# Optimization experiments

Hardware: AMD Instinct MI355X
Metric: run time of the kernel (lower is better)

The kernel has to match this reference:

```python
import jax, jax.numpy as jnp
import numpy as np

NEG_BIG = -2.0**32 + 1.0

def setup_inputs() -> dict:
    key = jax.random.key(0)
    ks = jax.random.split(key, 8)
    B, T, D = 4096, 200, 32
    H1, H2 = 80, 40
    s = lambda n: 1.0 / np.sqrt(n)
    return {
        "q": jax.random.normal(ks[0], (B, D), jnp.float32),
        "k": jax.random.normal(ks[1], (B, T, D), jnp.float32),
        "v": jax.random.normal(ks[2], (B, T, D), jnp.float32),
        "mask": jax.random.randint(ks[3], (B, T), 0, 2, jnp.int32),
        "Wq": jax.random.normal(ks[4], (D, D), jnp.float32) * s(D),
        "bq": jnp.zeros((D,), jnp.float32),
        "alpha": jnp.zeros((D,), jnp.float32),  # Keras PReLU default alpha=0
        "W1": jax.random.normal(ks[5], (4 * D, H1), jnp.float32) * s(4 * D),
        "b1": jnp.zeros((H1,), jnp.float32),
        "W2": jax.random.normal(ks[6], (H1, H2), jnp.float32) * s(H1),
        "b2": jnp.zeros((H2,), jnp.float32),
        "Wf": jax.random.normal(ks[7], (H2, 1), jnp.float32) * s(H2),
        "bf": jnp.zeros((1,), jnp.float32),
    }

def prelu(x, a):
    return jnp.where(x >= 0, x, a * x)

def reference(q, k, v, mask, Wq, bq, alpha, W1, b1, W2, b2, Wf, bf):
    # dense_q with PReLU activation: [B, D] -> [B, 32]
    qp = prelu(q @ Wq + bq, alpha)
    # tile query across history steps: [B, T, 32]
    qt = jnp.broadcast_to(qp[:, None, :], k.shape)
    # DIN attention features: [B, T, 4*32]
    info = jnp.concatenate([qt, k, qt - k, qt * k], axis=-1)
    info = jax.nn.sigmoid(info @ W1 + b1)
    info = jax.nn.sigmoid(info @ W2 + b2)
    logits = (info @ Wf + bf).squeeze(-1)  # [B, T]
    logits = jnp.where(mask == 0, jnp.full_like(logits, NEG_BIG), logits)
    att = jax.nn.softmax(logits, axis=-1)
    return att[:, None, :]  # [B, 1, T]
```

## Files before the change

kernel.cpp:

```cpp
#include <hip/hip_runtime.h>
#include <math.h>

typedef float f32x4 __attribute__((ext_vector_type(4)));
typedef _Float16 f16;
typedef f16 f16x8 __attribute__((ext_vector_type(8)));
typedef unsigned int u32;
typedef u32 u32x2 __attribute__((ext_vector_type(2)));

#define BB 4096
#define TT 200
#define DD 32
#define H1 80
#define H2 40
#define SLAB_W 104
#define LOG2E 1.44269504f

__device__ __align__(16) float g_BCj[DD * H1];
__device__ __align__(16) float g_Dj [DD * H1];
__device__ __align__(16) float g_ACj[DD * H1];
__device__ __align__(16) f16 g_w2h[9 * 64 * 8];

__device__ __forceinline__ float exp2_raw(float x) {
    float r;
    asm("v_exp_f32 %0, %1" : "=v"(r) : "v"(x));
    return r;
}
__device__ __forceinline__ float sig_pre(float a) {
    return __builtin_amdgcn_rcpf(1.f + exp2_raw(a));
}

__global__ void pack_kernel(const float* __restrict__ W1, const float* __restrict__ W2) {
    int idx = blockIdx.x * 256 + threadIdx.x;
    if (idx < DD * H1) {
        int kk = idx / H1, j = idx % H1;
        g_BCj[idx] = -LOG2E * (W1[(32 + kk) * H1 + j] - W1[(64 + kk) * H1 + j]);
        g_Dj [idx] = -LOG2E * W1[(96 + kk) * H1 + j];
        g_ACj[idx] = -LOG2E * (W1[kk * H1 + j] + W1[(64 + kk) * H1 + j]);
        return;
    }
    idx -= DD * H1;
    if (idx < 9 * 64 * 8) {
        int e = idx & 7, l = (idx >> 3) & 63, g = idx >> 9;
        int kt = g / 3, n = g % 3;
        int j   = kt * 32 + (l >> 4) * 8 + e;
        int col = n * 16 + (l & 15);
        float v = (j < H1 && col < H2) ? W2[j * H2 + col] : 0.f;
        g_w2h[idx] = (f16)(-LOG2E * v);
    }
}

__global__ __launch_bounds__(256) void din_mfma(
    const float* __restrict__ q, const float* __restrict__ k, const int* __restrict__ mask,
    const float* __restrict__ Wq, const float* __restrict__ bq, const float* __restrict__ alpha,
    const float* __restrict__ b1, const float* __restrict__ b2, const float* __restrict__ Wf,
    float* __restrict__ out)
{
    const int tid = threadIdx.x;
    const int wid = tid >> 6, l = tid & 63;
    const int l15 = l & 15, lg4 = l >> 4;
    const int r   = wid >> 1, s = wid & 1;
    const int b   = (blockIdx.x << 1) | r;

    __shared__ __align__(16) f16   slab[4][16][SLAB_W];
    __shared__ __align__(16) float qp_s[2][DD];
    __shared__ __align__(16) float u_s[2][H1];
    __shared__ __align__(16) float lgt[2][208];

    f16x8 W2r[9];
    #pragma unroll
    for (int g = 0; g < 9; ++g) W2r[g] = *(const f16x8*)(g_w2h + (g * 64 + l) * 8);

    const int* mrow = mask + (size_t)b * TT;
    int mk0 = mrow[l];
    int mk1 = mrow[64 + l];
    int mk2 = mrow[128 + l];
    int mk3 = (l < 8) ? mrow[192 + l] : 1;

    if (s == 0 && l < DD) {
        const float* qr = q + (size_t)b * DD;
        float acc = bq[l];
        #pragma unroll
        for (int e = 0; e < DD; ++e) acc += qr[e] * Wq[e * DD + l];
        float a = alpha[l];
        qp_s[r][l] = acc >= 0.f ? acc : a * acc;
    }
    {
        u32* z0 = (u32*)slab[wid];
        #pragma unroll
        for (int i = 0; i < 2; ++i) {
            int idx = i * 64 + l;
            z0[(idx >> 3) * 52 + 40 + (idx & 7)] = 0u;
        }
    }

    __syncthreads();
    const float* qp = qp_s[r];

    #pragma unroll
    for (int i = 0; i < 2; ++i) {
        int c = i * 64 + l;
        if (c < H1) {
            float acc = -LOG2E * b1[c];
            #pragma unroll
            for (int d = 0; d < DD; ++d) acc += qp[d] * g_ACj[d * H1 + c];
            u_s[r][c] = acc;
        }
    }
    f16x8 Bh[5];
    #pragma unroll
    for (int n = 0; n < 5; ++n) {
        #pragma unroll
        for (int e = 0; e < 8; ++e) {
            int kidx = lg4 * 8 + e;
            int j = n * 16 + l15;
            Bh[n][e] = (f16)(g_BCj[kidx * H1 + j] + qp[kidx] * g_Dj[kidx * H1 + j]);
        }
    }
    f32x4 b2r[3], wfr[3];
    #pragma unroll
    for (int n = 0; n < 3; ++n) {
        int c0 = n * 16 + lg4 * 4;
        if (c0 + 3 < H2) {
            f32x4 bv = *(const f32x4*)(b2 + c0);
            f32x4 wv = *(const f32x4*)(Wf + c0);
            #pragma unroll
            for (int e = 0; e < 4; ++e) { bv[e] *= -LOG2E; wv[e] *= LOG2E; }
            b2r[n] = bv;
            wfr[n] = wv;
        } else {
            b2r[n] = (f32x4){0.f, 0.f, 0.f, 0.f};
            wfr[n] = (f32x4){0.f, 0.f, 0.f, 0.f};
        }
    }
    f32x4 ur[5];
    #pragma unroll
    for (int n = 0; n < 5; ++n) ur[n] = *(const f32x4*)(&u_s[r][n * 16 + lg4 * 4]);

    const float* kb = k + (size_t)b * (TT * DD);
    f16 (*ws)[SLAB_W] = slab[wid];
    float* lg = lgt[r];

    f32x4 x0, x1;
    auto loadk = [&](int m) {
        int t = m * 16 + l15; if (t > TT - 1) t = TT - 1;
        const f32x4* kr = (const f32x4*)(kb + t * DD + lg4 * 8);
        x0 = kr[0]; x1 = kr[1];
    };

    auto l1_full = [&](int nload) {
        f16x8 Ah;
        #pragma unroll
        for (int e = 0; e < 4; ++e) {
            Ah[e]     = (f16)x0[e];
            Ah[e + 4] = (f16)x1[e];
        }
        if (nload >= 0) loadk(nload);
        #pragma unroll
        for (int n = 0; n < 5; ++n) {
            int j0 = n * 16 + lg4 * 4;
            f32x4 acc = ur[n];
            acc = __builtin_amdgcn_mfma_f32_16x16x32_f16(Bh[n], Ah, acc, 0, 0, 0);
            auto p01 = __builtin_amdgcn_cvt_pkrtz(sig_pre(acc[0]), sig_pre(acc[1]));
            auto p23 = __builtin_amdgcn_cvt_pkrtz(sig_pre(acc[2]), sig_pre(acc[3]));
            u32x2 w;
            w[0] = __builtin_bit_cast(u32, p01);
            w[1] = __builtin_bit_cast(u32, p23);
            *(u32x2*)(&ws[l15][j0]) = w;
        }
    };

    auto body = [&](int m) {
        f16x8 sh0 = *(const f16x8*)(&ws[l15][0 * 32 + lg4 * 8]);
        f16x8 sh1 = *(const f16x8*)(&ws[l15][1 * 32 + lg4 * 8]);
        f16x8 sh2 = *(const f16x8*)(&ws[l15][2 * 32 + lg4 * 8]);

        if (m + 2 < 13) l1_full(m + 4 < 13 ? m + 4 : -1);

        f32x4 a0 = {0.f,0.f,0.f,0.f}, a1 = {0.f,0.f,0.f,0.f}, a2 = {0.f,0.f,0.f,0.f};
        #pragma unroll
        for (int kt = 0; kt < 3; ++kt) {
            f16x8 sh = (kt == 0) ? sh0 : (kt == 1) ? sh1 : sh2;
            a0 = __builtin_amdgcn_mfma_f32_16x16x32_f16(W2r[kt * 3 + 0], sh, a0, 0, 0, 0);
            a1 = __builtin_amdgcn_mfma_f32_16x16x32_f16(W2r[kt * 3 + 1], sh, a1, 0, 0, 0);
            a2 = __builtin_amdgcn_mfma_f32_16x16x32_f16(W2r[kt * 3 + 2], sh, a2, 0, 0, 0);
        }

        float pn[3];
        #pragma unroll
        for (int n = 0; n < 3; ++n) {
            f32x4 av = (n == 0) ? a0 : (n == 1) ? a1 : a2;
            float t0 = wfr[n][0] * sig_pre(av[0] + b2r[n][0]);
            float t1 = wfr[n][1] * sig_pre(av[1] + b2r[n][1]);
            float t2 = wfr[n][2] * sig_pre(av[2] + b2r[n][2]);
            float t3 = wfr[n][3] * sig_pre(av[3] + b2r[n][3]);
            pn[n] = (t0 + t1) + (t2 + t3);
        }
        float p = (pn[0] + pn[1]) + pn[2];
        p += __shfl_xor(p, 16);
        p += __shfl_xor(p, 32);
        if (l < 16) lg[m * 16 + l15] = p;
    };

    loadk(s);
    l1_full(s + 2 < 13 ? s + 2 : -1);
    for (int m = s; m < 13; m += 2) body(m);

    __syncthreads();

    const float NEG = -4294967295.0f;
    float v0 = lg[l];        if (mk0 == 0) v0 = NEG;
    float v1 = lg[64 + l];   if (mk1 == 0) v1 = NEG;
    float v2 = lg[128 + l];  if (mk2 == 0) v2 = NEG;
    float v3 = -8589934590.0f;
    if (l < 8) { v3 = lg[192 + l]; if (mk3 == 0) v3 = NEG; }

    float mx = fmaxf(fmaxf(v0, v1), fmaxf(v2, v3));
    #pragma unroll
    for (int off = 32; off; off >>= 1) mx = fmaxf(mx, __shfl_xor(mx, off));

    float e0 = exp2_raw(v0 - mx), e1 = exp2_raw(v1 - mx);
    float e2 = exp2_raw(v2 - mx), e3 = exp2_raw(v3 - mx);
    float ssum = (e0 + e1) + (e2 + e3);
    #pragma unroll
    for (int off = 32; off; off >>= 1) ssum += __shfl_xor(ssum, off);

    float* orow = out + (size_t)b * TT;
    if (s == 0) {
        orow[l]      = e0 / ssum;
        orow[64 + l] = e1 / ssum;
    } else {
        orow[128 + l] = e2 / ssum;
        if (l < 8) orow[192 + l] = e3 / ssum;
    }
}

extern "C" void kernel_launch(void* const* d_in, const int* in_sizes, int n_in,
                              void* d_out, int out_size, void* d_ws, size_t ws_size,
                              hipStream_t stream) {
    const float* q     = (const float*)d_in[0];
    const float* k     = (const float*)d_in[1];
    const int*   mask  = (const int*)d_in[3];
    const float* Wq    = (const float*)d_in[4];
    const float* bq    = (const float*)d_in[5];
    const float* alpha = (const float*)d_in[6];
    const float* W1    = (const float*)d_in[7];
    const float* b1    = (const float*)d_in[8];
    const float* W2    = (const float*)d_in[9];
    const float* b2    = (const float*)d_in[10];
    const float* Wf    = (const float*)d_in[11];
    float* out = (float*)d_out;

    hipLaunchKernelGGL(pack_kernel, dim3((DD * H1 + 9 * 64 * 8 + 255) / 256), dim3(256),
                       0, stream, W1, W2);
    hipLaunchKernelGGL(din_mfma, dim3(BB / 2), dim3(256), 0, stream,
                       q, k, mask, Wq, bq, alpha, b1, b2, Wf, out);
}
```

Before: 58.60 us.

## Assign one wave per batch row with double-buffered slabs and LDS-resident W2

Each wave now owns a whole batch row, so a 256-thread block covers four rows and the grid is halved. The two-wave split per row is gone, which removes the cross-wave q projection sharing and the split softmax write. The W2 fragments and per-row layer-1 bias vectors move from registers into shared memory to relieve register pressure. Each wave interleaves two time tiles with double-buffered slabs to expose more independent MFMA and sigmoid work. The cost is extra LDS traffic for weights on every tile, and fewer blocks in flight.

```diff
diff --git a/kernel.cpp b/kernel.cpp
--- a/kernel.cpp
+++ b/kernel.cpp
@@ -58,17 +58,20 @@
     const int tid = threadIdx.x;
     const int wid = tid >> 6, l = tid & 63;
     const int l15 = l & 15, lg4 = l >> 4;
-    const int r   = wid >> 1, s = wid & 1;
-    const int b   = (blockIdx.x << 1) | r;
-
-    __shared__ __align__(16) f16   slab[4][16][SLAB_W];
-    __shared__ __align__(16) float qp_s[2][DD];
-    __shared__ __align__(16) float u_s[2][H1];
-    __shared__ __align__(16) float lgt[2][208];
-
-    f16x8 W2r[9];
-    #pragma unroll
-    for (int g = 0; g < 9; ++g) W2r[g] = *(const f16x8*)(g_w2h + (g * 64 + l) * 8);
+    const int b   = (blockIdx.x << 2) | wid;
+
+    __shared__ __align__(16) f16   slab[4][2][16][SLAB_W];
+    __shared__ __align__(16) f16   w2h_s[9 * 64 * 8];
+    __shared__ __align__(16) float u_s[4][H1];
+    __shared__ __align__(16) float lgt[4][208];
+    float* qp = lgt[wid];
+
+    {
+        const u32* src = (const u32*)g_w2h;
+        u32* dst = (u32*)w2h_s;
+        #pragma unroll
+        for (int i = 0; i < 9; ++i) dst[i * 256 + tid] = src[i * 256 + tid];
+    }
 
     const int* mrow = mask + (size_t)b * TT;
     int mk0 = mrow[l];
@@ -76,25 +79,25 @@
     int mk2 = mrow[128 + l];
     int mk3 = (l < 8) ? mrow[192 + l] : 1;
 
-    if (s == 0 && l < DD) {
+    if (l < DD) {
         const float* qr = q + (size_t)b * DD;
         float acc = bq[l];
         #pragma unroll
         for (int e = 0; e < DD; ++e) acc += qr[e] * Wq[e * DD + l];
         float a = alpha[l];
-        qp_s[r][l] = acc >= 0.f ? acc : a * acc;
+        qp[l] = acc >= 0.f ? acc : a * acc;
     }
     {
-        u32* z0 = (u32*)slab[wid];
+        u32* z0 = (u32*)slab[wid][0];
+        u32* z1 = (u32*)slab[wid][1];
         #pragma unroll
         for (int i = 0; i < 2; ++i) {
             int idx = i * 64 + l;
-            z0[(idx >> 3) * 52 + 40 + (idx & 7)] = 0u;
-        }
-    }
-
-    __syncthreads();
-    const float* qp = qp_s[r];
+            int off = (idx >> 3) * 52 + 40 + (idx & 7);
+            z0[off] = 0u;
+            z1[off] = 0u;
+        }
+    }
 
     #pragma unroll
     for (int i = 0; i < 2; ++i) {
@@ -103,7 +106,7 @@
             float acc = -LOG2E * b1[c];
             #pragma unroll
             for (int d = 0; d < DD; ++d) acc += qp[d] * g_ACj[d * H1 + c];
-            u_s[r][c] = acc;
+            u_s[wid][c] = acc;
         }
     }
     f16x8 Bh[5];
@@ -132,59 +135,55 @@
             wfr[n] = (f32x4){0.f, 0.f, 0.f, 0.f};
         }
     }
-    f32x4 ur[5];
-    #pragma unroll
-    for (int n = 0; n < 5; ++n) ur[n] = *(const f32x4*)(&u_s[r][n * 16 + lg4 * 4]);
+
+    __syncthreads();
 
     const float* kb = k + (size_t)b * (TT * DD);
-    f16 (*ws)[SLAB_W] = slab[wid];
-    float* lg = lgt[r];
-
-    f32x4 x0, x1;
-    auto loadk = [&](int m) {
+    f16 (*ws0)[SLAB_W] = slab[wid][0];
+    f16 (*ws1)[SLAB_W] = slab[wid][1];
+    float* lg = lgt[wid];
+
+    f32x4 x0, x1, x2, x3;
+    auto loadk = [&](int m, f32x4& a, f32x4& c) {
         int t = m * 16 + l15; if (t > TT - 1) t = TT - 1;
         const f32x4* kr = (const f32x4*)(kb + t * DD + lg4 * 8);
-        x0 = kr[0]; x1 = kr[1];
+        a = kr[0]; c = kr[1];
     };
 
-    auto l1_full = [&](int nload) {
+    auto l1_full = [&](f16 (*wbuf)[SLAB_W], f32x4& xa, f32x4& xb, int nload) {
         f16x8 Ah;
         #pragma unroll
         for (int e = 0; e < 4; ++e) {
-            Ah[e]     = (f16)x0[e];
-            Ah[e + 4] = (f16)x1[e];
-        }
-        if (nload >= 0) loadk(nload);
+            Ah[e]     = (f16)xa[e];
+            Ah[e + 4] = (f16)xb[e];
+        }
+        if (nload >= 0) loadk(nload, xa, xb);
         #pragma unroll
         for (int n = 0; n < 5; ++n) {
             int j0 = n * 16 + lg4 * 4;
-            f32x4 acc = ur[n];
+            f32x4 acc = *(const f32x4*)(&u_s[wid][j0]);
             acc = __builtin_amdgcn_mfma_f32_16x16x32_f16(Bh[n], Ah, acc, 0, 0, 0);
             auto p01 = __builtin_amdgcn_cvt_pkrtz(sig_pre(acc[0]), sig_pre(acc[1]));
             auto p23 = __builtin_amdgcn_cvt_pkrtz(sig_pre(acc[2]), sig_pre(acc[3]));
             u32x2 w;
             w[0] = __builtin_bit_cast(u32, p01);
             w[1] = __builtin_bit_cast(u32, p23);
-            *(u32x2*)(&ws[l15][j0]) = w;
+            *(u32x2*)(&wbuf[l15][j0]) = w;
         }
     };
 
-    auto body = [&](int m) {
-        f16x8 sh0 = *(const f16x8*)(&ws[l15][0 * 32 + lg4 * 8]);
-        f16x8 sh1 = *(const f16x8*)(&ws[l15][1 * 32 + lg4 * 8]);
-        f16x8 sh2 = *(const f16x8*)(&ws[l15][2 * 32 + lg4 * 8]);
-
-        if (m + 2 < 13) l1_full(m + 4 < 13 ? m + 4 : -1);
-
+    auto l2_one = [&](int m, f16x8 sh0, f16x8 sh1, f16x8 sh2) {
         f32x4 a0 = {0.f,0.f,0.f,0.f}, a1 = {0.f,0.f,0.f,0.f}, a2 = {0.f,0.f,0.f,0.f};
         #pragma unroll
         for (int kt = 0; kt < 3; ++kt) {
+            f16x8 w0 = *(const f16x8*)(w2h_s + ((kt * 3 + 0) * 64 + l) * 8);
+            f16x8 w1 = *(const f16x8*)(w2h_s + ((kt * 3 + 1) * 64 + l) * 8);
+            f16x8 w2 = *(const f16x8*)(w2h_s + ((kt * 3 + 2) * 64 + l) * 8);
             f16x8 sh = (kt == 0) ? sh0 : (kt == 1) ? sh1 : sh2;
-            a0 = __builtin_amdgcn_mfma_f32_16x16x32_f16(W2r[kt * 3 + 0], sh, a0, 0, 0, 0);
-            a1 = __builtin_amdgcn_mfma_f32_16x16x32_f16(W2r[kt * 3 + 1], sh, a1, 0, 0, 0);
-            a2 = __builtin_amdgcn_mfma_f32_16x16x32_f16(W2r[kt * 3 + 2], sh, a2, 0, 0, 0);
-        }
-
+            a0 = __builtin_amdgcn_mfma_f32_16x16x32_f16(w0, sh, a0, 0, 0, 0);
+            a1 = __builtin_amdgcn_mfma_f32_16x16x32_f16(w1, sh, a1, 0, 0, 0);
+            a2 = __builtin_amdgcn_mfma_f32_16x16x32_f16(w2, sh, a2, 0, 0, 0);
+        }
         float pn[3];
         #pragma unroll
         for (int n = 0; n < 3; ++n) {
@@ -201,11 +200,26 @@
         if (l < 16) lg[m * 16 + l15] = p;
     };
 
-    loadk(s);
-    l1_full(s + 2 < 13 ? s + 2 : -1);
-    for (int m = s; m < 13; m += 2) body(m);
-
-    __syncthreads();
+    loadk(0, x0, x1);
+    loadk(1, x2, x3);
+    l1_full(ws0, x0, x1, 2);
+    l1_full(ws1, x2, x3, 3);
+
+    for (int m = 0; m < 13; m += 2) {
+        f16x8 sA0 = *(const f16x8*)(&ws0[l15][0 * 32 + lg4 * 8]);
+        f16x8 sA1 = *(const f16x8*)(&ws0[l15][1 * 32 + lg4 * 8]);
+        f16x8 sA2 = *(const f16x8*)(&ws0[l15][2 * 32 + lg4 * 8]);
+        f16x8 sB0, sB1, sB2;
+        if (m + 1 < 13) {
+            sB0 = *(const f16x8*)(&ws1[l15][0 * 32 + lg4 * 8]);
+            sB1 = *(const f16x8*)(&ws1[l15][1 * 32 + lg4 * 8]);
+            sB2 = *(const f16x8*)(&ws1[l15][2 * 32 + lg4 * 8]);
+        }
+        if (m + 2 < 13) l1_full(ws0, x0, x1, (m + 4 < 13) ? m + 4 : -1);
+        if (m + 3 < 13) l1_full(ws1, x2, x3, (m + 5 < 13) ? m + 5 : -1);
+        l2_one(m, sA0, sA1, sA2);
+        if (m + 1 < 13) l2_one(m + 1, sB0, sB1, sB2);
+    }
 
     const float NEG = -4294967295.0f;
     float v0 = lg[l];        if (mk0 == 0) v0 = NEG;
@@ -225,13 +239,10 @@
     for (int off = 32; off; off >>= 1) ssum += __shfl_xor(ssum, off);
 
     float* orow = out + (size_t)b * TT;
-    if (s == 0) {
-        orow[l]      = e0 / ssum;
-        orow[64 + l] = e1 / ssum;
-    } else {
-        orow[128 + l] = e2 / ssum;
-        if (l < 8) orow[192 + l] = e3 / ssum;
-    }
+    orow[l]       = e0 / ssum;
+    orow[64 + l]  = e1 / ssum;
+    orow[128 + l] = e2 / ssum;
+    if (l < 8) orow[192 + l] = e3 / ssum;
 }
 
 extern "C" void kernel_launch(void* const* d_in, const int* in_sizes, int n_in,
@@ -252,6 +263,6 @@
 
     hipLaunchKernelGGL(pack_kernel, dim3((DD * H1 + 9 * 64 * 8 + 255) / 256), dim3(256),
                        0, stream, W1, W2);
-    hipLaunchKernelGGL(din_mfma, dim3(BB / 2), dim3(256), 0, stream,
+    hipLaunchKernelGGL(din_mfma, dim3(BB / 4), dim3(256), 0, stream,
                        q, k, mask, Wq, bq, alpha, b1, b2, Wf, out);
 }
```

After: 51.68 us. -11.8%, faster.

## Assign one batch row per wavefront and pre-pack weights for vector loads

Applied to the files above, without the earlier changes.

Each wavefront now handles a whole batch row instead of two wavefronts splitting one row's time tiles. This removes both block-wide __syncthreads and leaves each wave independent, though every wave now does the full per-row prologue (query projection, u vector, Bh build). The pack kernel now also writes a transposed Wq and lane-ordered W1 fragments, so those prologue dot products use float4 loads instead of strided scalar loads. The grid shrinks to BB/4 blocks, and per-wave serial work per block goes up.

```diff
diff --git a/kernel.cpp b/kernel.cpp
--- a/kernel.cpp
+++ b/kernel.cpp
@@ -15,10 +15,11 @@
 #define SLAB_W 104
 #define LOG2E 1.44269504f
 
-__device__ __align__(16) float g_BCj[DD * H1];
-__device__ __align__(16) float g_Dj [DD * H1];
-__device__ __align__(16) float g_ACj[DD * H1];
-__device__ __align__(16) f16 g_w2h[9 * 64 * 8];
+__device__ __align__(16) float g_wqt[DD * DD];
+__device__ __align__(16) float g_act[H1 * DD];
+__device__ __align__(16) float g_bcf[5 * 64 * 8];
+__device__ __align__(16) float g_df [5 * 64 * 8];
+__device__ __align__(16) f16   g_w2h[9 * 64 * 8];
 
 __device__ __forceinline__ float exp2_raw(float x) {
     float r;
@@ -29,16 +30,30 @@
     return __builtin_amdgcn_rcpf(1.f + exp2_raw(a));
 }
 
-__global__ void pack_kernel(const float* __restrict__ W1, const float* __restrict__ W2) {
+__global__ void pack_kernel(const float* __restrict__ W1, const float* __restrict__ W2,
+                            const float* __restrict__ Wq) {
     int idx = blockIdx.x * 256 + threadIdx.x;
-    if (idx < DD * H1) {
-        int kk = idx / H1, j = idx % H1;
-        g_BCj[idx] = -LOG2E * (W1[(32 + kk) * H1 + j] - W1[(64 + kk) * H1 + j]);
-        g_Dj [idx] = -LOG2E * W1[(96 + kk) * H1 + j];
-        g_ACj[idx] = -LOG2E * (W1[kk * H1 + j] + W1[(64 + kk) * H1 + j]);
+    if (idx < DD * DD) {
+        int col = idx / DD, e = idx % DD;
+        g_wqt[idx] = Wq[e * DD + col];
         return;
     }
-    idx -= DD * H1;
+    idx -= DD * DD;
+    if (idx < H1 * DD) {
+        int c = idx / DD, d = idx % DD;
+        g_act[idx] = -LOG2E * (W1[d * H1 + c] + W1[(64 + d) * H1 + c]);
+        return;
+    }
+    idx -= H1 * DD;
+    if (idx < 5 * 64 * 8) {
+        int e = idx & 7, l = (idx >> 3) & 63, n = idx >> 9;
+        int kidx = (l >> 4) * 8 + e;
+        int j = n * 16 + (l & 15);
+        g_bcf[idx] = -LOG2E * (W1[(32 + kidx) * H1 + j] - W1[(64 + kidx) * H1 + j]);
+        g_df [idx] = -LOG2E * W1[(96 + kidx) * H1 + j];
+        return;
+    }
+    idx -= 5 * 64 * 8;
     if (idx < 9 * 64 * 8) {
         int e = idx & 7, l = (idx >> 3) & 63, g = idx >> 9;
         int kt = g / 3, n = g % 3;
@@ -51,20 +66,19 @@
 
 __global__ __launch_bounds__(256) void din_mfma(
     const float* __restrict__ q, const float* __restrict__ k, const int* __restrict__ mask,
-    const float* __restrict__ Wq, const float* __restrict__ bq, const float* __restrict__ alpha,
+    const float* __restrict__ bq, const float* __restrict__ alpha,
     const float* __restrict__ b1, const float* __restrict__ b2, const float* __restrict__ Wf,
     float* __restrict__ out)
 {
     const int tid = threadIdx.x;
     const int wid = tid >> 6, l = tid & 63;
     const int l15 = l & 15, lg4 = l >> 4;
-    const int r   = wid >> 1, s = wid & 1;
-    const int b   = (blockIdx.x << 1) | r;
+    const int b   = (blockIdx.x << 2) | wid;
 
     __shared__ __align__(16) f16   slab[4][16][SLAB_W];
-    __shared__ __align__(16) float qp_s[2][DD];
-    __shared__ __align__(16) float u_s[2][H1];
-    __shared__ __align__(16) float lgt[2][208];
+    __shared__ __align__(16) float u_s[4][H1];
+    __shared__ __align__(16) float lgt[4][208];
+    float* qp = lgt[wid];
 
     f16x8 W2r[9];
     #pragma unroll
@@ -76,13 +90,17 @@
     int mk2 = mrow[128 + l];
     int mk3 = (l < 8) ? mrow[192 + l] : 1;
 
-    if (s == 0 && l < DD) {
-        const float* qr = q + (size_t)b * DD;
+    if (l < DD) {
+        const f32x4* qv = (const f32x4*)(q + (size_t)b * DD);
+        const f32x4* wv = (const f32x4*)(g_wqt + l * DD);
         float acc = bq[l];
         #pragma unroll
-        for (int e = 0; e < DD; ++e) acc += qr[e] * Wq[e * DD + l];
-        float a = alpha[l];
-        qp_s[r][l] = acc >= 0.f ? acc : a * acc;
+        for (int i = 0; i < 8; ++i) {
+            f32x4 a = qv[i], w = wv[i];
+            acc += (a[0] * w[0] + a[1] * w[1]) + (a[2] * w[2] + a[3] * w[3]);
+        }
+        float al = alpha[l];
+        qp[l] = acc >= 0.f ? acc : al * acc;
     }
     {
         u32* z0 = (u32*)slab[wid];
@@ -93,27 +111,36 @@
         }
     }
 
-    __syncthreads();
-    const float* qp = qp_s[r];
+    f32x4 qp4[8];
+    #pragma unroll
+    for (int j = 0; j < 8; ++j) qp4[j] = *(const f32x4*)(&qp[j * 4]);
+    f32x4 qpa = *(const f32x4*)(&qp[lg4 * 8]);
+    f32x4 qpb = *(const f32x4*)(&qp[lg4 * 8 + 4]);
 
     #pragma unroll
     for (int i = 0; i < 2; ++i) {
         int c = i * 64 + l;
         if (c < H1) {
+            const f32x4* av = (const f32x4*)(g_act + c * DD);
             float acc = -LOG2E * b1[c];
             #pragma unroll
-            for (int d = 0; d < DD; ++d) acc += qp[d] * g_ACj[d * H1 + c];
-            u_s[r][c] = acc;
+            for (int j = 0; j < 8; ++j) {
+                f32x4 a = av[j], p = qp4[j];
+                acc += (a[0] * p[0] + a[1] * p[1]) + (a[2] * p[2] + a[3] * p[3]);
+            }
+            u_s[wid][c] = acc;
         }
     }
     f16x8 Bh[5];
     #pragma unroll
     for (int n = 0; n < 5; ++n) {
-        #pragma unroll
-        for (int e = 0; e < 8; ++e) {
-            int kidx = lg4 * 8 + e;
-            int j = n * 16 + l15;
-            Bh[n][e] = (f16)(g_BCj[kidx * H1 + j] + qp[kidx] * g_Dj[kidx * H1 + j]);
+        const f32x4* bv = (const f32x4*)(g_bcf + (n * 64 + l) * 8);
+        const f32x4* dv = (const f32x4*)(g_df  + (n * 64 + l) * 8);
+        f32x4 b0 = bv[0], b1v = bv[1], d0 = dv[0], d1 = dv[1];
+        #pragma unroll
+        for (int e = 0; e < 4; ++e) {
+            Bh[n][e]     = (f16)(b0[e]  + qpa[e] * d0[e]);
+            Bh[n][e + 4] = (f16)(b1v[e] + qpb[e] * d1[e]);
         }
     }
     f32x4 b2r[3], wfr[3];
@@ -134,11 +161,11 @@
     }
     f32x4 ur[5];
     #pragma unroll
-    for (int n = 0; n < 5; ++n) ur[n] = *(const f32x4*)(&u_s[r][n * 16 + lg4 * 4]);
+    for (int n = 0; n < 5; ++n) ur[n] = *(const f32x4*)(&u_s[wid][n * 16 + lg4 * 4]);
 
     const float* kb = k + (size_t)b * (TT * DD);
     f16 (*ws)[SLAB_W] = slab[wid];
-    float* lg = lgt[r];
+    float* lg = lgt[wid];
 
     f32x4 x0, x1;
     auto loadk = [&](int m) {
@@ -174,7 +201,7 @@
         f16x8 sh1 = *(const f16x8*)(&ws[l15][1 * 32 + lg4 * 8]);
         f16x8 sh2 = *(const f16x8*)(&ws[l15][2 * 32 + lg4 * 8]);
 
-        if (m + 2 < 13) l1_full(m + 4 < 13 ? m + 4 : -1);
+        if (m < 12) l1_full(m < 11 ? m + 2 : -1);
 
         f32x4 a0 = {0.f,0.f,0.f,0.f}, a1 = {0.f,0.f,0.f,0.f}, a2 = {0.f,0.f,0.f,0.f};
         #pragma unroll
@@ -201,11 +228,9 @@
         if (l < 16) lg[m * 16 + l15] = p;
     };
 
-    loadk(s);
-    l1_full(s + 2 < 13 ? s + 2 : -1);
-    for (int m = s; m < 13; m += 2) body(m);
-
-    __syncthreads();
+    loadk(0);
+    l1_full(1);
+    for (int m = 0; m < 13; ++m) body(m);
 
     const float NEG = -4294967295.0f;
     float v0 = lg[l];        if (mk0 == 0) v0 = NEG;
@@ -225,13 +250,10 @@
     for (int off = 32; off; off >>= 1) ssum += __shfl_xor(ssum, off);
 
     float* orow = out + (size_t)b * TT;
-    if (s == 0) {
-        orow[l]      = e0 / ssum;
-        orow[64 + l] = e1 / ssum;
-    } else {
-        orow[128 + l] = e2 / ssum;
-        if (l < 8) orow[192 + l] = e3 / ssum;
-    }
+    orow[l]       = e0 / ssum;
+    orow[64 + l]  = e1 / ssum;
+    orow[128 + l] = e2 / ssum;
+    if (l < 8) orow[192 + l] = e3 / ssum;
 }
 
 extern "C" void kernel_launch(void* const* d_in, const int* in_sizes, int n_in,
@@ -250,8 +272,7 @@
     const float* Wf    = (const float*)d_in[11];
     float* out = (float*)d_out;
 
-    hipLaunchKernelGGL(pack_kernel, dim3((DD * H1 + 9 * 64 * 8 + 255) / 256), dim3(256),
-                       0, stream, W1, W2);
-    hipLaunchKernelGGL(din_mfma, dim3(BB / 2), dim3(256), 0, stream,
-                       q, k, mask, Wq, bq, alpha, b1, b2, Wf, out);
-}
+    hipLaunchKernelGGL(pack_kernel, dim3(52), dim3(256), 0, stream, W1, W2, Wq);
+    hipLaunchKernelGGL(din_mfma, dim3(BB / 4), dim3(256), 0, stream,
+                       q, k, mask, bq, alpha, b1, b2, Wf, out);
+}
```

New measurement: 51.00 us. 1.15x faster.
